# Kernel optimization log

Hardware: AMD Instinct MI355X
Metric: run time of the kernel (lower is better)

## Reference

```python
import jax, jax.numpy as jnp
import numpy as np

SLOPE = 25.0  # snntorch surrogate.fast_sigmoid default slope
THR = 1.0
BETA = 0.5
NUM_HEADS = 8

@jax.custom_vjp
def spike(u):
    # forward: heaviside; backward: fast-sigmoid surrogate
    return (u > 0).astype(u.dtype)

def _spike_fwd(u):
    return (u > 0).astype(u.dtype), u

def _spike_bwd(u, g):
    return (g / (SLOPE * jnp.abs(u) + 1.0) ** 2,)

spike.defvjp(_spike_fwd, _spike_bwd)

def lif(inp, mem):
    # snntorch Leaky, reset_mechanism='subtract': reset from previous mem (detached)
    reset = jax.lax.stop_gradient((mem > THR).astype(mem.dtype))
    mem_new = BETA * mem + inp - reset * THR
    spk = spike(mem_new - THR)
    return spk, mem_new

def conv1x1(x, W):
    # nn.Conv2d(C,C,1,bias=False): pure channel matmul
    return jnp.einsum('bihw,oi->bohw', x, W)

def setup_inputs():
    key = jax.random.key(0)
    ks = jax.random.split(key, 5)
    B, C, H, W = 8, 256, 64, 64
    x = jax.random.normal(ks[0], (B, C, H, W), jnp.float32)
    z = jnp.zeros((B, C, H, W), jnp.float32)
    s = 1.0 / np.sqrt(C)
    Wq = jax.random.normal(ks[1], (C, C), jnp.float32) * s
    Wk = jax.random.normal(ks[2], (C, C), jnp.float32) * s
    Wv = jax.random.normal(ks[3], (C, C), jnp.float32) * s
    Wo = jax.random.normal(ks[4], (C, C), jnp.float32) * s
    gamma = jnp.ones((C,), jnp.float32)
    beta_bn = jnp.zeros((C,), jnp.float32)
    return {'x': x, 'q_mem': z, 'k_mem': z, 'v_mem': z,
            'Wq': Wq, 'Wk': Wk, 'Wv': Wv, 'Wo': Wo,
            'gamma': gamma, 'beta_bn': beta_bn}

def reference(x, q_mem, k_mem, v_mem, Wq, Wk, Wv, Wo, gamma, beta_bn):
    B, C, H, W = x.shape
    N = H * W
    hd = C // NUM_HEADS
    scale = hd ** -0.5

    q_spk, q_mem_n = lif(conv1x1(x, Wq), q_mem)
    k_spk, k_mem_n = lif(conv1x1(x, Wk), k_mem)
    v_spk, v_mem_n = lif(conv1x1(x, Wv), v_mem)

    # bipolar spikes in {-1,+1}, reshape to (B, h, N, d)
    def to_heads(s):
        t = (2.0 * s - 1.0).reshape(B, NUM_HEADS, hd, N)
        return jnp.transpose(t, (0, 1, 3, 2))

    q = jax.nn.elu(to_heads(q_spk)) + 1.0
    k = jax.nn.elu(to_heads(k_spk)) + 1.0
    v = to_heads(v_spk)

    kv = jnp.einsum('bhnd,bhne->bhde', k, v)            # (B,h,d,d)
    out = jnp.einsum('bhnd,bhde->bhne', q, kv) * scale  # (B,h,N,d)
    k_sum = jnp.sum(k, axis=2)                          # (B,h,d)
    denom = jnp.einsum('bhnd,bhd->bhn', q, k_sum) + 1e-6
    out = out / denom[..., None]

    out = jnp.transpose(out, (0, 1, 3, 2)).reshape(B, C, H, W)
    out = conv1x1(out, Wo)

    # BatchNorm2d, training mode (biased batch stats), eps=1e-5
    mean = jnp.mean(out, axis=(0, 2, 3), keepdims=True)
    var = jnp.var(out, axis=(0, 2, 3), keepdims=True)
    out = (out - mean) / jnp.sqrt(var + 1e-5)
    out = out * gamma[None, :, None, None] + beta_bn[None, :, None, None]

    return (out, q_mem_n, k_mem_n, v_mem_n)
```

## Files before the change

kernel.cpp:

```cpp
#include <hip/hip_runtime.h>

#define B_ 8
#define C_ 256
#define N_ 4096
#define HD_ 32

#define ALPHA_ 0.36787944117144233f
#define BETAS_ (2.0f - ALPHA_)
#define SCALE_ 0.17677669529663687f

typedef _Float16 f16;
typedef _Float16 f16x8 __attribute__((ext_vector_type(8)));
typedef float f32x4 __attribute__((ext_vector_type(4)));
typedef unsigned long long u64;
typedef __attribute__((address_space(3))) f16 lds_f16;

#define MFMA(a,b,c) __builtin_amdgcn_mfma_f32_16x16x32_f16((a),(b),(c),0,0,0)

#define GLDS(g, l) __builtin_amdgcn_global_load_lds( \
    (const __attribute__((address_space(1))) void*)(g), \
    (__attribute__((address_space(3))) void*)(l), 16, 0, 0)

#define DSR(dst, off) asm volatile("ds_read_b128 %0, %1" : "=v"(dst) : "v"(off))

#define GLA(dst, ptr, ofs) asm volatile( \
    "global_load_dwordx4 %0, %1, off offset:%c2" \
    : "=v"(dst) : "v"(ptr), "i"(ofs))

template<int N> __device__ __forceinline__ void wait_vmcnt() {
    if constexpr (N == 0)       asm volatile("s_waitcnt vmcnt(0)" ::: "memory");
    else if constexpr (N == 2)  asm volatile("s_waitcnt vmcnt(2)" ::: "memory");
    else if constexpr (N == 4)  asm volatile("s_waitcnt vmcnt(4)" ::: "memory");
    else if constexpr (N == 6)  asm volatile("s_waitcnt vmcnt(6)" ::: "memory");
    else if constexpr (N == 8)  asm volatile("s_waitcnt vmcnt(8)" ::: "memory");
    else if constexpr (N == 12) asm volatile("s_waitcnt vmcnt(12)" ::: "memory");
    else if constexpr (N == 16) asm volatile("s_waitcnt vmcnt(16)" ::: "memory");
}

__global__ __launch_bounds__(256) void transpose_split(
    const float* __restrict__ x, f16* __restrict__ XTh, f16* __restrict__ XTl)
{
    __shared__ float tile[32][257];
    int t = threadIdx.x;
    int b = blockIdx.z, i0 = blockIdx.y * 32, n0 = blockIdx.x * 256;
    const float* src = x + ((size_t)b * C_ + i0) * N_ + n0;
    int r = t >> 3, c0 = (t & 7) * 32;
    #pragma unroll
    for (int q = 0; q < 8; ++q) {
        float4 v = *reinterpret_cast<const float4*>(src + (size_t)r * N_ + c0 + q * 4);
        tile[r][c0 + q*4 + 0] = v.x; tile[r][c0 + q*4 + 1] = v.y;
        tile[r][c0 + q*4 + 2] = v.z; tile[r][c0 + q*4 + 3] = v.w;
    }
    __syncthreads();
    size_t ob = ((size_t)b * N_ + n0 + t) * C_ + i0;
    #pragma unroll
    for (int q = 0; q < 4; ++q) {
        f16x8 hv, lv;
        #pragma unroll
        for (int j = 0; j < 8; ++j) {
            float v = tile[q*8 + j][t];
            f16 h = (f16)v;
            hv[j] = h;
            lv[j] = (f16)(v - (float)h);
        }
        *reinterpret_cast<f16x8*>(XTh + ob + q*8) = hv;
        *reinterpret_cast<f16x8*>(XTl + ob + q*8) = lv;
    }
}

__global__ __launch_bounds__(256) void weight_split(
    const float* __restrict__ Wq, const float* __restrict__ Wk,
    const float* __restrict__ Wv, const float* __restrict__ Wo,
    f16* __restrict__ Wch, f16* __restrict__ Wcl)
{
    int idx4 = (blockIdx.x * 256 + threadIdx.x) * 4;
    int o = idx4 >> 8, i = idx4 & 255;
    const float* src = (o < 256) ? (Wq + (size_t)o * 256)
                     : (o < 512) ? (Wk + (size_t)(o - 256) * 256)
                     : (o < 768) ? (Wv + (size_t)(o - 512) * 256)
                                 : (Wo + (size_t)(o - 768) * 256);
    float4 v = *reinterpret_cast<const float4*>(src + i);
    f16 h0 = (f16)v.x, h1 = (f16)v.y, h2 = (f16)v.z, h3 = (f16)v.w;
    f16 hh[4] = { h0, h1, h2, h3 };
    f16 ll[4] = { (f16)(v.x - (float)h0), (f16)(v.y - (float)h1),
                  (f16)(v.z - (float)h2), (f16)(v.w - (float)h3) };
    *reinterpret_cast<uint2*>(Wch + idx4) = *reinterpret_cast<uint2*>(hh);
    *reinterpret_cast<uint2*>(Wcl + idx4) = *reinterpret_cast<uint2*>(ll);
}

template<bool LIF, bool FULLP>
__global__ __launch_bounds__(256, 2) void mfma_gemm(
    const f16* __restrict__ Wch, const f16* __restrict__ Wcl,
    const f16* __restrict__ Bh,  const f16* __restrict__ Bl,
    const float* __restrict__ mq, const float* __restrict__ mk2,
    const float* __restrict__ mv,
    float* __restrict__ o0, float* __restrict__ o1, float* __restrict__ o2,
    u64* __restrict__ rowAll, float2* __restrict__ part)
{
    constexpr int SLOTS = FULLP ? 1024 : 512;
    constexpr int NGL   = FULLP ? 4 : 2;
    constexpr int NA    = FULLP ? 8 : 4;

    int gid = blockIdx.x;
    int b = gid & 7, slot = gid >> 3;
    int conv, oTi, nt;
    if (LIF) { conv = slot % 3; int rest = slot / 3; oTi = rest & 1; nt = rest >> 1; }
    else     { conv = 0;        oTi = slot & 1;      nt = slot >> 1; }
    int wRow0 = (LIF ? conv * 256 : 768) + oTi * 128;
    int chOut0 = oTi * 128;
    int nT = nt * 128;

    const float* memP = nullptr; float* outP; u64* rowP = nullptr;
    if (LIF) {
        memP = (conv == 0) ? mq : (conv == 1) ? mk2 : mv;
        outP = (conv == 0) ? o0 : (conv == 1) ? o1 : o2;
        rowP = rowAll + (size_t)conv * (8 * 256 * 64);
    } else outP = o0;

    __shared__ __align__(16) f16 smem[3][SLOTS * 8];

    int t = threadIdx.x;
    int wid = t >> 6, lane = t & 63;
    int wm = wid >> 1, wn = wid & 1;
    int lr = lane & 15, g = lane >> 4;

    const f16* gB[NGL];
    #pragma unroll
    for (int i = 0; i < NGL; ++i) {
        int s = i * 256 + t;
        int sp = s & 511;
        int r = sp >> 2, c = (sp & 3) ^ ((r >> 1) & 3);
        const f16* plane = (s < 512) ? Bh : Bl;
        gB[i] = plane + ((size_t)b * N_ + nT + r) * 256 + c * 8;
    }

    const f16* aPh[4]; const f16* aPl[4];
    #pragma unroll
    for (int m = 0; m < 4; ++m) {
        int off = (wRow0 + wm * 64 + m * 16 + lr) * 256 + g * 8;
        aPh[m] = Wch + off;
        aPl[m] = Wcl + off;
    }

    unsigned lbase = (unsigned)(size_t)(lds_f16*)&smem[0][0];
    unsigned offB[4];
    #pragma unroll
    for (int n = 0; n < 4; ++n) {
        int r = wn * 64 + n * 16 + lr;
        offB[n] = (unsigned)((r * 4 + (g ^ ((r >> 1) & 3))) * 16);
    }

    f32x4 acc[4][4];
    #pragma unroll
    for (int m = 0; m < 4; ++m)
        #pragma unroll
        for (int n = 0; n < 4; ++n) acc[m][n] = (f32x4){0.f, 0.f, 0.f, 0.f};

    f16x8 aH[2][4], aL[2][4];

    #pragma unroll
    for (int i = 0; i < NGL; ++i) GLDS(gB[i], &smem[0][(i * 256 + t) * 8]);
    #pragma unroll
    for (int m = 0; m < 4; ++m) {
        GLA(aH[0][m], aPh[m], 0);
        if (FULLP) GLA(aL[0][m], aPl[m], 0);
    }
    #pragma unroll
    for (int i = 0; i < NGL; ++i) GLDS(gB[i] + 32, &smem[1][(i * 256 + t) * 8]);
    wait_vmcnt<NGL>();
    __builtin_amdgcn_s_barrier();
    __builtin_amdgcn_sched_barrier(0);

#define GEMM_STEP(KS) do { \
    constexpr int ks = (KS); \
    constexpr int cur = ks & 1, nxt = (ks + 1) & 1; \
     \
    const unsigned base = lbase + (unsigned)((ks % 3) * (SLOTS * 16)); \
    f16x8 bhf[4], blf[4]; \
    _Pragma("unroll") \
    for (int n = 0; n < 4; ++n) { \
        DSR(bhf[n], base + offB[n]); \
        if (FULLP) DSR(blf[n], base + offB[n] + 8192); \
    } \
    __builtin_amdgcn_sched_barrier(0); \
     \
    if constexpr (ks < 7) { \
        _Pragma("unroll") \
        for (int m = 0; m < 4; ++m) { \
            GLA(aH[nxt][m], aPh[m], (ks + 1) * 64); \
            if (FULLP) GLA(aL[nxt][m], aPl[m], (ks + 1) * 64); \
        } \
    } \
    __builtin_amdgcn_sched_barrier(0); \
     \
    if constexpr (ks < 6) { \
        _Pragma("unroll") \
        for (int i = 0; i < NGL; ++i) \
            GLDS(gB[i] + (ks + 2) * 32, &smem[(ks + 2) % 3][(i * 256 + t) * 8]); \
    } \
    __builtin_amdgcn_sched_barrier(0); \
    asm volatile("s_waitcnt lgkmcnt(0)" ::: "memory"); \
    __builtin_amdgcn_sched_barrier(0); \
     \
    wait_vmcnt<(ks <= 5) ? (2 * NGL + NA) : (ks == 6 ? (NGL + NA) : 0)>(); \
    __builtin_amdgcn_sched_barrier(0); \
    _Pragma("unroll") \
    for (int n = 0; n < 4; ++n) \
        _Pragma("unroll") \
        for (int m = 0; m < 4; ++m) { \
            acc[m][n] = MFMA(aH[cur][m], bhf[n], acc[m][n]); \
            if (FULLP) { \
                acc[m][n] = MFMA(aH[cur][m], blf[n], acc[m][n]); \
                acc[m][n] = MFMA(aL[cur][m], bhf[n], acc[m][n]); \
            } \
        } \
    __builtin_amdgcn_sched_barrier(0); \
    if constexpr (ks < 7) { \
         \
        wait_vmcnt<(ks <= 5) ? (NA + NGL) : NA>(); \
        __builtin_amdgcn_s_barrier(); \
        __builtin_amdgcn_sched_barrier(0); \
    } \
} while (0)

    GEMM_STEP(0); GEMM_STEP(1); GEMM_STEP(2); GEMM_STEP(3);
    GEMM_STEP(4); GEMM_STEP(5); GEMM_STEP(6); GEMM_STEP(7);
#undef GEMM_STEP

    if (LIF) {
        #pragma unroll
        for (int m = 0; m < 4; ++m) {
            int oLoc = chOut0 + wm * 64 + m * 16 + g * 4;
            u64 rw0 = 0, rw1 = 0, rw2 = 0, rw3 = 0;
            #pragma unroll
            for (int n = 0; n < 4; ++n) {
                int nn = nT + wn * 64 + n * 16 + lr;
                #pragma unroll
                for (int r = 0; r < 4; ++r) {
                    size_t idx = ((size_t)b * C_ + oLoc + r) * N_ + nn;
                    float mm = memP[idx];
                    float v = 0.5f * mm + acc[m][n][r] - (mm > 1.0f ? 1.0f : 0.0f);
                    outP[idx] = v;
                    u64 bl = __ballot(v > 1.0f);
                    u64 fld = ((bl >> (g * 16)) & 0xFFFFull) << (n * 16);
                    if (r == 0) rw0 |= fld; else if (r == 1) rw1 |= fld;
                    else if (r == 2) rw2 |= fld; else rw3 |= fld;
                }
            }
            if (lr == 0) {
                size_t rb = ((size_t)b * 256 + oLoc) * 64 + (nt * 2 + wn);
                rowP[rb]       = rw0;
                rowP[rb + 64]  = rw1;
                rowP[rb + 128] = rw2;
                rowP[rb + 192] = rw3;
            }
        }
    } else {
        #pragma unroll
        for (int m = 0; m < 4; ++m) {
            #pragma unroll
            for (int r = 0; r < 4; ++r) {
                int ch = chOut0 + wm * 64 + m * 16 + g * 4 + r;
                float s1 = 0.f, s2 = 0.f;
                #pragma unroll
                for (int n = 0; n < 4; ++n) {
                    int nn = nT + wn * 64 + n * 16 + lr;
                    size_t idx = ((size_t)b * C_ + ch) * N_ + nn;
                    float v = acc[m][n][r];
                    outP[idx] = v;
                    s1 += v; s2 += v * v;
                }
                #pragma unroll
                for (int w = 1; w < 16; w <<= 1) {
                    s1 += __shfl_xor(s1, w);
                    s2 += __shfl_xor(s2, w);
                }
                if (lr == 0)
                    part[((size_t)ch * 8 + b) * 64 + nt * 2 + wn] = make_float2(s1, s2);
            }
        }
    }
}

__global__ __launch_bounds__(256) void kv_kernel(
    const u64* __restrict__ krow, const u64* __restrict__ vrow,
    float* __restrict__ kvp, float* __restrict__ ksump)
{
    int bh = blockIdx.x;
    int b = bh >> 3, h = bh & 7;
    __shared__ u64 kr[32][65], vr[32][65];
    __shared__ float ck[32], cv[32];
    int t = threadIdx.x;
    {
        size_t base = ((size_t)b * 256 + h * HD_) * 64;
        #pragma unroll
        for (int j = 0; j < 8; ++j) {
            int idx = t * 8 + j;
            int d = idx >> 6, w = idx & 63;
            kr[d][w] = krow[base + idx];
            vr[d][w] = vrow[base + idx];
        }
    }
    __syncthreads();

    if (t < 32) {
        int c = 0;
        for (int w = 0; w < 64; ++w) c += __popcll(kr[t][w]);
        ck[t] = (float)c;
    } else if (t < 64) {
        int dd = t - 32, c = 0;
        for (int w = 0; w < 64; ++w) c += __popcll(vr[dd][w]);
        cv[dd] = (float)c;
    }
    __syncthreads();

    int d = t >> 3, e0 = (t & 7) * 4;
    #pragma unroll
    for (int j = 0; j < 4; ++j) {
        int e = e0 + j, P = 0;
        for (int w = 0; w < 64; ++w) P += __popcll(kr[d][w] & vr[e][w]);
        float skv = 2.0f * (float)P - ck[d];
        float sv  = 2.0f * cv[e] - 4096.0f;
        kvp[(size_t)bh * 1024 + d * 32 + e] = ALPHA_ * sv + BETAS_ * skv;
    }
    if ((t & 7) == 0)
        ksump[bh * 32 + d] = ALPHA_ * 4096.0f + BETAS_ * ck[d];
}

__global__ __launch_bounds__(256) void att_kernel(
    const u64* __restrict__ qrow, const float* __restrict__ kvp,
    const float* __restrict__ ksump, f16* __restrict__ ATh)
{
    int bh = blockIdx.y; int b = bh >> 3, h = bh & 7;
    int n0 = blockIdx.x * 256;

    __shared__ u64 qw[32][5];
    int t = threadIdx.x;
    if (t < 128) {
        int d2 = t >> 2, w4 = t & 3;
        qw[d2][w4] = qrow[((size_t)b * 256 + h * HD_ + d2) * 64 + (n0 >> 6) + w4];
    }
    __syncthreads();

    float q[32];
    #pragma unroll
    for (int d2 = 0; d2 < 32; ++d2)
        q[d2] = ((qw[d2][t >> 6] >> (t & 63)) & 1) ? 2.0f : ALPHA_;

    const float* ksb = ksump + bh * 32;
    float den = 1e-6f;
    #pragma unroll
    for (int d2 = 0; d2 < 32; ++d2) den += q[d2] * ksb[d2];
    float rden = SCALE_ / den;

    const float* kvb = kvp + (size_t)bh * 1024;
    size_t ob = ((size_t)b * N_ + n0 + t) * C_ + h * HD_;
    #pragma unroll
    for (int qq = 0; qq < 4; ++qq) {
        f16x8 hv;
        #pragma unroll
        for (int j = 0; j < 8; ++j) {
            int e = qq * 8 + j;
            float num = 0.0f;
            #pragma unroll
            for (int d2 = 0; d2 < 32; ++d2) num += q[d2] * kvb[d2 * 32 + e];
            hv[j] = (f16)(num * rden);
        }
        *reinterpret_cast<f16x8*>(ATh + ob + qq * 8) = hv;
    }
}

__global__ __launch_bounds__(256) void bn_stats(
    const float2* __restrict__ part, float* __restrict__ stats)
{
    int o = blockIdx.x, t = threadIdx.x;
    float2 a = part[(size_t)o * 512 + t];
    float2 c = part[(size_t)o * 512 + 256 + t];
    double s = (double)a.x + (double)c.x;
    double ss = (double)a.y + (double)c.y;
    __shared__ double rs[256], rss[256];
    rs[t] = s; rss[t] = ss;
    __syncthreads();
    for (int st = 128; st > 0; st >>= 1) {
        if (t < st) { rs[t] += rs[t + st]; rss[t] += rss[t + st]; }
        __syncthreads();
    }
    if (t == 0) {
        double mean = rs[0] / 32768.0;
        double var  = rss[0] / 32768.0 - mean * mean;
        stats[o * 2 + 0] = (float)mean;
        stats[o * 2 + 1] = (float)(1.0 / sqrt(var + 1e-5));
    }
}

__global__ __launch_bounds__(256) void bn_apply(
    float* __restrict__ out, const float* __restrict__ stats,
    const float* __restrict__ gamma, const float* __restrict__ beta)
{
    size_t i = ((size_t)blockIdx.x * 256 + threadIdx.x) * 4;
    int o = (int)((i >> 12) & 255);
    float m = stats[o * 2], r = stats[o * 2 + 1];
    float g = gamma[o] * r;
    float c = beta[o] - m * g;
    float4 v = *reinterpret_cast<float4*>(&out[i]);
    v.x = v.x * g + c; v.y = v.y * g + c;
    v.z = v.z * g + c; v.w = v.w * g + c;
    *reinterpret_cast<float4*>(&out[i]) = v;
}

extern "C" void kernel_launch(void* const* d_in, const int* in_sizes, int n_in,
                              void* d_out, int out_size, void* d_ws, size_t ws_size,
                              hipStream_t stream)
{
    (void)in_sizes; (void)n_in; (void)out_size; (void)ws_size;

    const float* x     = (const float*)d_in[0];
    const float* qmem  = (const float*)d_in[1];
    const float* kmem  = (const float*)d_in[2];
    const float* vmem  = (const float*)d_in[3];
    const float* Wq    = (const float*)d_in[4];
    const float* Wk    = (const float*)d_in[5];
    const float* Wv    = (const float*)d_in[6];
    const float* Wo    = (const float*)d_in[7];
    const float* gamma = (const float*)d_in[8];
    const float* beta  = (const float*)d_in[9];

    const size_t TSZ = (size_t)B_ * C_ * N_;
    float* out0 = (float*)d_out;
    float* outq = out0 + TSZ;
    float* outk = outq + TSZ;
    float* outv = outk + TSZ;

    const size_t RSZ = (size_t)8 * 256 * 64;
    char* w = (char*)d_ws;
    f16* XTh = (f16*)w;           w += TSZ * 2;
    f16* XTl = (f16*)w;           w += TSZ * 2;
    f16* ATh = (f16*)w;           w += TSZ * 2;
    f16* Wch = (f16*)w;           w += 1024 * 256 * 2;
    f16* Wcl = (f16*)w;           w += 1024 * 256 * 2;
    u64* rowm = (u64*)w;          w += 3 * RSZ * 8;
    float2* part = (float2*)w;    w += 256 * 8 * 64 * 8;
    float* kvp   = (float*)w;     w += 64 * 1024 * 4;
    float* ksump = (float*)w;     w += 64 * 32 * 4;
    float* stats = (float*)w;     w += 256 * 2 * 4;

    dim3 blk(256);

    transpose_split<<<dim3(16, 8, 8), blk, 0, stream>>>(x, XTh, XTl);
    weight_split<<<dim3(256), blk, 0, stream>>>(Wq, Wk, Wv, Wo, Wch, Wcl);

    mfma_gemm<true, true><<<dim3(1536), blk, 0, stream>>>(
        Wch, Wcl, XTh, XTl, qmem, kmem, vmem, outq, outk, outv, rowm, nullptr);

    kv_kernel<<<dim3(64), blk, 0, stream>>>(rowm + RSZ, rowm + 2 * RSZ, kvp, ksump);

    att_kernel<<<dim3(16, 64), blk, 0, stream>>>(rowm, kvp, ksump, ATh);

    mfma_gemm<false, false><<<dim3(512), blk, 0, stream>>>(
        Wch, Wcl, ATh, ATh, nullptr, nullptr, nullptr, out0, nullptr, nullptr,
        nullptr, part);

    bn_stats<<<dim3(256), blk, 0, stream>>>(part, stats);
    bn_apply<<<dim3(8192), blk, 0, stream>>>(out0, stats, gamma, beta);
}
```

Measured before the change: 177.7 us.

## Give each wave private LDS B tiles to remove block barriers in GEMM

The GEMM main loop now has each wave load its own 64-row slice of the B operand into a wave-private, double-buffered LDS region, using a new XOR swizzle that interleaves the hi and lo planes. Because no wave reads another wave's data, the per-step s_barrier is dropped and the only synchronization left is vmcnt waits. The A-fragment and B prefetch now issue after the MFMAs for the step, two steps ahead. The cost is that B rows are duplicated across the wm wave pairs, which doubles global-to-LDS traffic and changes LDS size and occupancy.

```diff
diff --git a/kernel.cpp b/kernel.cpp
--- a/kernel.cpp
+++ b/kernel.cpp
@@ -29,11 +29,7 @@
 
 template<int N> __device__ __forceinline__ void wait_vmcnt() {
     if constexpr (N == 0)       asm volatile("s_waitcnt vmcnt(0)" ::: "memory");
-    else if constexpr (N == 2)  asm volatile("s_waitcnt vmcnt(2)" ::: "memory");
-    else if constexpr (N == 4)  asm volatile("s_waitcnt vmcnt(4)" ::: "memory");
-    else if constexpr (N == 6)  asm volatile("s_waitcnt vmcnt(6)" ::: "memory");
     else if constexpr (N == 8)  asm volatile("s_waitcnt vmcnt(8)" ::: "memory");
-    else if constexpr (N == 12) asm volatile("s_waitcnt vmcnt(12)" ::: "memory");
     else if constexpr (N == 16) asm volatile("s_waitcnt vmcnt(16)" ::: "memory");
 }
 
@@ -97,8 +93,9 @@
     float* __restrict__ o0, float* __restrict__ o1, float* __restrict__ o2,
     u64* __restrict__ rowAll, float2* __restrict__ part)
 {
-    constexpr int SLOTS = FULLP ? 1024 : 512;
-    constexpr int NGL   = FULLP ? 4 : 2;
+    constexpr int CH    = FULLP ? 8 : 4;
+    constexpr int SLOTB = FULLP ? 8192 : 4096;
+    constexpr int NGL   = FULLP ? 8 : 4;
     constexpr int NA    = FULLP ? 8 : 4;
 
     int gid = blockIdx.x;
@@ -117,21 +114,27 @@
         rowP = rowAll + (size_t)conv * (8 * 256 * 64);
     } else outP = o0;
 
-    __shared__ __align__(16) f16 smem[3][SLOTS * 8];
+    __shared__ __align__(16) char smem[4 * 2 * SLOTB];
 
     int t = threadIdx.x;
     int wid = t >> 6, lane = t & 63;
     int wm = wid >> 1, wn = wid & 1;
     int lr = lane & 15, g = lane >> 4;
 
+    const unsigned wbase = (unsigned)(wid * 2 * SLOTB);
+
     const f16* gB[NGL];
     #pragma unroll
     for (int i = 0; i < NGL; ++i) {
-        int s = i * 256 + t;
-        int sp = s & 511;
-        int r = sp >> 2, c = (sp & 3) ^ ((r >> 1) & 3);
-        const f16* plane = (s < 512) ? Bh : Bl;
-        gB[i] = plane + ((size_t)b * N_ + nT + r) * 256 + c * 8;
+        int s = i * 64 + lane;
+        int r, dc;
+        if (FULLP) { r = s >> 3; dc = (s & 7) ^ (r & 7); }
+        else       { r = s >> 2; dc = (s & 3) ^ (r & 3); }
+        const f16* plane;
+        int kc;
+        if (FULLP) { plane = (dc & 1) ? Bl : Bh; kc = dc >> 1; }
+        else       { plane = Bh;                 kc = dc; }
+        gB[i] = plane + ((size_t)b * N_ + nT + wn * 64 + r) * 256 + kc * 8;
     }
 
     const f16* aPh[4]; const f16* aPl[4];
@@ -142,12 +145,17 @@
         aPl[m] = Wcl + off;
     }
 
-    unsigned lbase = (unsigned)(size_t)(lds_f16*)&smem[0][0];
-    unsigned offB[4];
+    unsigned lbase = (unsigned)(size_t)(lds_f16*)&smem[0];
+    unsigned offBh[4], offBl[4];
     #pragma unroll
     for (int n = 0; n < 4; ++n) {
-        int r = wn * 64 + n * 16 + lr;
-        offB[n] = (unsigned)((r * 4 + (g ^ ((r >> 1) & 3))) * 16);
+        int rB = n * 16 + lr;
+        if (FULLP) {
+            offBh[n] = (unsigned)(rB * 128 + (((2 * g)     ^ (rB & 7)) * 16));
+            offBl[n] = (unsigned)(rB * 128 + (((2 * g + 1) ^ (rB & 7)) * 16));
+        } else {
+            offBh[n] = (unsigned)(rB * 64 + ((g ^ (rB & 3)) * 16));
+        }
     }
 
     f32x4 acc[4][4];
@@ -159,50 +167,35 @@
     f16x8 aH[2][4], aL[2][4];
 
     #pragma unroll
-    for (int i = 0; i < NGL; ++i) GLDS(gB[i], &smem[0][(i * 256 + t) * 8]);
+    for (int i = 0; i < NGL; ++i)
+        GLDS(gB[i], &smem[wbase + i * 1024]);
     #pragma unroll
     for (int m = 0; m < 4; ++m) {
         GLA(aH[0][m], aPh[m], 0);
         if (FULLP) GLA(aL[0][m], aPl[m], 0);
     }
     #pragma unroll
-    for (int i = 0; i < NGL; ++i) GLDS(gB[i] + 32, &smem[1][(i * 256 + t) * 8]);
-    wait_vmcnt<NGL>();
-    __builtin_amdgcn_s_barrier();
+    for (int i = 0; i < NGL; ++i)
+        GLDS(gB[i] + 32, &smem[wbase + SLOTB + i * 1024]);
+    #pragma unroll
+    for (int m = 0; m < 4; ++m) {
+        GLA(aH[1][m], aPh[m], 64);
+        if (FULLP) GLA(aL[1][m], aPl[m], 64);
+    }
+    wait_vmcnt<NGL + NA>();
     __builtin_amdgcn_sched_barrier(0);
 
 #define GEMM_STEP(KS) do { \
     constexpr int ks = (KS); \
-    constexpr int cur = ks & 1, nxt = (ks + 1) & 1; \
-     \
-    const unsigned base = lbase + (unsigned)((ks % 3) * (SLOTS * 16)); \
+    constexpr int cur = ks & 1; \
+    const unsigned bb = lbase + wbase + (unsigned)(cur * SLOTB); \
     f16x8 bhf[4], blf[4]; \
     _Pragma("unroll") \
     for (int n = 0; n < 4; ++n) { \
-        DSR(bhf[n], base + offB[n]); \
-        if (FULLP) DSR(blf[n], base + offB[n] + 8192); \
+        DSR(bhf[n], bb + offBh[n]); \
+        if (FULLP) DSR(blf[n], bb + offBl[n]); \
     } \
-    __builtin_amdgcn_sched_barrier(0); \
-     \
-    if constexpr (ks < 7) { \
-        _Pragma("unroll") \
-        for (int m = 0; m < 4; ++m) { \
-            GLA(aH[nxt][m], aPh[m], (ks + 1) * 64); \
-            if (FULLP) GLA(aL[nxt][m], aPl[m], (ks + 1) * 64); \
-        } \
-    } \
-    __builtin_amdgcn_sched_barrier(0); \
-     \
-    if constexpr (ks < 6) { \
-        _Pragma("unroll") \
-        for (int i = 0; i < NGL; ++i) \
-            GLDS(gB[i] + (ks + 2) * 32, &smem[(ks + 2) % 3][(i * 256 + t) * 8]); \
-    } \
-    __builtin_amdgcn_sched_barrier(0); \
     asm volatile("s_waitcnt lgkmcnt(0)" ::: "memory"); \
-    __builtin_amdgcn_sched_barrier(0); \
-     \
-    wait_vmcnt<(ks <= 5) ? (2 * NGL + NA) : (ks == 6 ? (NGL + NA) : 0)>(); \
     __builtin_amdgcn_sched_barrier(0); \
     _Pragma("unroll") \
     for (int n = 0; n < 4; ++n) \
@@ -215,12 +208,20 @@
             } \
         } \
     __builtin_amdgcn_sched_barrier(0); \
-    if constexpr (ks < 7) { \
-         \
-        wait_vmcnt<(ks <= 5) ? (NA + NGL) : NA>(); \
-        __builtin_amdgcn_s_barrier(); \
-        __builtin_amdgcn_sched_barrier(0); \
+    if constexpr (ks < 6) { \
+        _Pragma("unroll") \
+        for (int i = 0; i < NGL; ++i) \
+            GLDS(gB[i] + (ks + 2) * 32, &smem[wbase + cur * SLOTB + i * 1024]); \
+        _Pragma("unroll") \
+        for (int m = 0; m < 4; ++m) { \
+            GLA(aH[cur][m], aPh[m], (ks + 2) * 64); \
+            if (FULLP) GLA(aL[cur][m], aPl[m], (ks + 2) * 64); \
+        } \
     } \
+    __builtin_amdgcn_sched_barrier(0); \
+    if constexpr (ks < 6)      wait_vmcnt<NGL + NA>();  \
+    else if constexpr (ks == 6) wait_vmcnt<0>();         \
+    __builtin_amdgcn_sched_barrier(0); \
 } while (0)
 
     GEMM_STEP(0); GEMM_STEP(1); GEMM_STEP(2); GEMM_STEP(3);
```

Result: slower. 194.6 us (+9.5%).

## Stage weight tiles through LDS with 64x128 tiles and double buffering

Applied to the files above, without the earlier changes.

The GEMM kernels now use 64x128 output tiles instead of 128x128, which doubles the grid and raises the launch bound to three blocks per CU. Weight (A) fragments are no longer loaded per wave from global memory into registers; they are copied into LDS with global_load_lds next to the B tile, using an XOR swizzle. The three-stage B ring becomes a two-stage double buffer with a full vmcnt(0) wait before each barrier. This should cut register pressure and redundant weight loads and allow more occupancy, but each B tile is now fetched twice as often and less load latency is overlapped with compute.

```diff
diff --git a/kernel.cpp b/kernel.cpp
--- a/kernel.cpp
+++ b/kernel.cpp
@@ -23,18 +23,10 @@
 
 #define DSR(dst, off) asm volatile("ds_read_b128 %0, %1" : "=v"(dst) : "v"(off))
 
-#define GLA(dst, ptr, ofs) asm volatile( \
-    "global_load_dwordx4 %0, %1, off offset:%c2" \
-    : "=v"(dst) : "v"(ptr), "i"(ofs))
-
 template<int N> __device__ __forceinline__ void wait_vmcnt() {
     if constexpr (N == 0)       asm volatile("s_waitcnt vmcnt(0)" ::: "memory");
-    else if constexpr (N == 2)  asm volatile("s_waitcnt vmcnt(2)" ::: "memory");
-    else if constexpr (N == 4)  asm volatile("s_waitcnt vmcnt(4)" ::: "memory");
+    else if constexpr (N == 3)  asm volatile("s_waitcnt vmcnt(3)" ::: "memory");
     else if constexpr (N == 6)  asm volatile("s_waitcnt vmcnt(6)" ::: "memory");
-    else if constexpr (N == 8)  asm volatile("s_waitcnt vmcnt(8)" ::: "memory");
-    else if constexpr (N == 12) asm volatile("s_waitcnt vmcnt(12)" ::: "memory");
-    else if constexpr (N == 16) asm volatile("s_waitcnt vmcnt(16)" ::: "memory");
 }
 
 __global__ __launch_bounds__(256) void transpose_split(
@@ -89,7 +81,7 @@
 }
 
 template<bool LIF, bool FULLP>
-__global__ __launch_bounds__(256, 2) void mfma_gemm(
+__global__ __launch_bounds__(256, 3) void mfma_gemm(
     const f16* __restrict__ Wch, const f16* __restrict__ Wcl,
     const f16* __restrict__ Bh,  const f16* __restrict__ Bl,
     const float* __restrict__ mq, const float* __restrict__ mk2,
@@ -97,17 +89,20 @@
     float* __restrict__ o0, float* __restrict__ o1, float* __restrict__ o2,
     u64* __restrict__ rowAll, float2* __restrict__ part)
 {
-    constexpr int SLOTS = FULLP ? 1024 : 512;
-    constexpr int NGL   = FULLP ? 4 : 2;
-    constexpr int NA    = FULLP ? 8 : 4;
+    constexpr int CHA   = FULLP ? 8 : 4;
+    constexpr int CHL   = FULLP ? 3 : 2;
+    constexpr int ABYTE = 64 * CHA * 16;
+    constexpr int SLOTS = 192 * CHA;
+    constexpr int SLOTB = SLOTS * 16;
+    constexpr int NGL   = SLOTS / 256;
 
     int gid = blockIdx.x;
     int b = gid & 7, slot = gid >> 3;
     int conv, oTi, nt;
-    if (LIF) { conv = slot % 3; int rest = slot / 3; oTi = rest & 1; nt = rest >> 1; }
-    else     { conv = 0;        oTi = slot & 1;      nt = slot >> 1; }
-    int wRow0 = (LIF ? conv * 256 : 768) + oTi * 128;
-    int chOut0 = oTi * 128;
+    if (LIF) { conv = slot % 3; int rest = slot / 3; oTi = rest & 3; nt = rest >> 2; }
+    else     { conv = 0;        oTi = slot & 3;      nt = slot >> 2; }
+    int wRow0 = (LIF ? conv * 256 : 768) + oTi * 64;
+    int chOut0 = oTi * 64;
     int nT = nt * 128;
 
     const float* memP = nullptr; float* outP; u64* rowP = nullptr;
@@ -117,107 +112,100 @@
         rowP = rowAll + (size_t)conv * (8 * 256 * 64);
     } else outP = o0;
 
-    __shared__ __align__(16) f16 smem[3][SLOTS * 8];
+    __shared__ __align__(16) char smem[2][SLOTB];
 
     int t = threadIdx.x;
     int wid = t >> 6, lane = t & 63;
     int wm = wid >> 1, wn = wid & 1;
     int lr = lane & 15, g = lane >> 4;
 
-    const f16* gB[NGL];
+    const f16* gS[NGL];
     #pragma unroll
     for (int i = 0; i < NGL; ++i) {
         int s = i * 256 + t;
-        int sp = s & 511;
-        int r = sp >> 2, c = (sp & 3) ^ ((r >> 1) & 3);
-        const f16* plane = (s < 512) ? Bh : Bl;
-        gB[i] = plane + ((size_t)b * N_ + nT + r) * 256 + c * 8;
-    }
-
-    const f16* aPh[4]; const f16* aPl[4];
-    #pragma unroll
-    for (int m = 0; m < 4; ++m) {
-        int off = (wRow0 + wm * 64 + m * 16 + lr) * 256 + g * 8;
-        aPh[m] = Wch + off;
-        aPl[m] = Wcl + off;
+        const f16* gp;
+        if (s < 64 * CHA) {
+            int r = s >> CHL, dcl = (s & (CHA - 1)) ^ (r & (CHA - 1));
+            int kc = FULLP ? (dcl & 3) : dcl;
+            const f16* pl = (FULLP && (dcl >> 2)) ? Wcl : Wch;
+            gp = pl + (size_t)(wRow0 + r) * 256 + kc * 8;
+        } else {
+            int s2 = s - 64 * CHA;
+            int r = s2 >> CHL, dcl = (s2 & (CHA - 1)) ^ (r & (CHA - 1));
+            int kc = FULLP ? (dcl & 3) : dcl;
+            const f16* pl = (FULLP && (dcl >> 2)) ? Bl : Bh;
+            gp = pl + ((size_t)b * N_ + nT + r) * 256 + kc * 8;
+        }
+        gS[i] = gp;
     }
 
     unsigned lbase = (unsigned)(size_t)(lds_f16*)&smem[0][0];
-    unsigned offB[4];
+    unsigned offAh[2], offAl[2], offBh[4], offBl[4];
+    #pragma unroll
+    for (int m = 0; m < 2; ++m) {
+        int rA = wm * 32 + m * 16 + lr;
+        offAh[m] = (unsigned)((rA * CHA + (g ^ (rA & (CHA - 1)))) * 16);
+        if (FULLP)
+            offAl[m] = (unsigned)((rA * CHA + ((g + 4) ^ (rA & (CHA - 1)))) * 16);
+    }
     #pragma unroll
     for (int n = 0; n < 4; ++n) {
-        int r = wn * 64 + n * 16 + lr;
-        offB[n] = (unsigned)((r * 4 + (g ^ ((r >> 1) & 3))) * 16);
-    }
-
-    f32x4 acc[4][4];
-    #pragma unroll
-    for (int m = 0; m < 4; ++m)
+        int rB = wn * 64 + n * 16 + lr;
+        offBh[n] = (unsigned)(ABYTE + (rB * CHA + (g ^ (rB & (CHA - 1)))) * 16);
+        if (FULLP)
+            offBl[n] = (unsigned)(ABYTE + (rB * CHA + ((g + 4) ^ (rB & (CHA - 1)))) * 16);
+    }
+
+    f32x4 acc[2][4];
+    #pragma unroll
+    for (int m = 0; m < 2; ++m)
         #pragma unroll
         for (int n = 0; n < 4; ++n) acc[m][n] = (f32x4){0.f, 0.f, 0.f, 0.f};
 
-    f16x8 aH[2][4], aL[2][4];
-
-    #pragma unroll
-    for (int i = 0; i < NGL; ++i) GLDS(gB[i], &smem[0][(i * 256 + t) * 8]);
-    #pragma unroll
-    for (int m = 0; m < 4; ++m) {
-        GLA(aH[0][m], aPh[m], 0);
-        if (FULLP) GLA(aL[0][m], aPl[m], 0);
-    }
-    #pragma unroll
-    for (int i = 0; i < NGL; ++i) GLDS(gB[i] + 32, &smem[1][(i * 256 + t) * 8]);
-    wait_vmcnt<NGL>();
+    #pragma unroll
+    for (int i = 0; i < NGL; ++i)
+        GLDS(gS[i], &smem[0][(i * 256 + t) * 16]);
+    wait_vmcnt<0>();
     __builtin_amdgcn_s_barrier();
     __builtin_amdgcn_sched_barrier(0);
 
 #define GEMM_STEP(KS) do { \
     constexpr int ks = (KS); \
-    constexpr int cur = ks & 1, nxt = (ks + 1) & 1; \
-     \
-    const unsigned base = lbase + (unsigned)((ks % 3) * (SLOTS * 16)); \
-    f16x8 bhf[4], blf[4]; \
-    _Pragma("unroll") \
-    for (int n = 0; n < 4; ++n) { \
-        DSR(bhf[n], base + offB[n]); \
-        if (FULLP) DSR(blf[n], base + offB[n] + 8192); \
-    } \
-    __builtin_amdgcn_sched_barrier(0); \
+    constexpr int cur = ks & 1; \
      \
     if constexpr (ks < 7) { \
         _Pragma("unroll") \
-        for (int m = 0; m < 4; ++m) { \
-            GLA(aH[nxt][m], aPh[m], (ks + 1) * 64); \
-            if (FULLP) GLA(aL[nxt][m], aPl[m], (ks + 1) * 64); \
-        } \
+        for (int i = 0; i < NGL; ++i) \
+            GLDS(gS[i] + (ks + 1) * 32, &smem[cur ^ 1][(i * 256 + t) * 16]); \
     } \
     __builtin_amdgcn_sched_barrier(0); \
-     \
-    if constexpr (ks < 6) { \
-        _Pragma("unroll") \
-        for (int i = 0; i < NGL; ++i) \
-            GLDS(gB[i] + (ks + 2) * 32, &smem[(ks + 2) % 3][(i * 256 + t) * 8]); \
+    const unsigned bb = lbase + (unsigned)(cur * SLOTB); \
+    f16x8 ah[2], al[2], bhf[4], blf[4]; \
+    _Pragma("unroll") \
+    for (int m = 0; m < 2; ++m) { \
+        DSR(ah[m], bb + offAh[m]); \
+        if (FULLP) DSR(al[m], bb + offAl[m]); \
     } \
-    __builtin_amdgcn_sched_barrier(0); \
+    _Pragma("unroll") \
+    for (int n = 0; n < 4; ++n) { \
+        DSR(bhf[n], bb + offBh[n]); \
+        if (FULLP) DSR(blf[n], bb + offBl[n]); \
+    } \
     asm volatile("s_waitcnt lgkmcnt(0)" ::: "memory"); \
-    __builtin_amdgcn_sched_barrier(0); \
-     \
-    wait_vmcnt<(ks <= 5) ? (2 * NGL + NA) : (ks == 6 ? (NGL + NA) : 0)>(); \
     __builtin_amdgcn_sched_barrier(0); \
     _Pragma("unroll") \
     for (int n = 0; n < 4; ++n) \
         _Pragma("unroll") \
-        for (int m = 0; m < 4; ++m) { \
-            acc[m][n] = MFMA(aH[cur][m], bhf[n], acc[m][n]); \
+        for (int m = 0; m < 2; ++m) { \
+            acc[m][n] = MFMA(ah[m], bhf[n], acc[m][n]); \
             if (FULLP) { \
-                acc[m][n] = MFMA(aH[cur][m], blf[n], acc[m][n]); \
-                acc[m][n] = MFMA(aL[cur][m], bhf[n], acc[m][n]); \
+                acc[m][n] = MFMA(ah[m], blf[n], acc[m][n]); \
+                acc[m][n] = MFMA(al[m], bhf[n], acc[m][n]); \
             } \
         } \
     __builtin_amdgcn_sched_barrier(0); \
     if constexpr (ks < 7) { \
-         \
-        wait_vmcnt<(ks <= 5) ? (NA + NGL) : NA>(); \
+        wait_vmcnt<0>();                  \
         __builtin_amdgcn_s_barrier(); \
         __builtin_amdgcn_sched_barrier(0); \
     } \
@@ -229,8 +217,8 @@
 
     if (LIF) {
         #pragma unroll
-        for (int m = 0; m < 4; ++m) {
-            int oLoc = chOut0 + wm * 64 + m * 16 + g * 4;
+        for (int m = 0; m < 2; ++m) {
+            int oLoc = chOut0 + wm * 32 + m * 16 + g * 4;
             u64 rw0 = 0, rw1 = 0, rw2 = 0, rw3 = 0;
             #pragma unroll
             for (int n = 0; n < 4; ++n) {
@@ -257,10 +245,10 @@
         }
     } else {
         #pragma unroll
-        for (int m = 0; m < 4; ++m) {
+        for (int m = 0; m < 2; ++m) {
             #pragma unroll
             for (int r = 0; r < 4; ++r) {
-                int ch = chOut0 + wm * 64 + m * 16 + g * 4 + r;
+                int ch = chOut0 + wm * 32 + m * 16 + g * 4 + r;
                 float s1 = 0.f, s2 = 0.f;
                 #pragma unroll
                 for (int n = 0; n < 4; ++n) {
@@ -449,14 +437,14 @@
     transpose_split<<<dim3(16, 8, 8), blk, 0, stream>>>(x, XTh, XTl);
     weight_split<<<dim3(256), blk, 0, stream>>>(Wq, Wk, Wv, Wo, Wch, Wcl);
 
-    mfma_gemm<true, true><<<dim3(1536), blk, 0, stream>>>(
+    mfma_gemm<true, true><<<dim3(3072), blk, 0, stream>>>(
         Wch, Wcl, XTh, XTl, qmem, kmem, vmem, outq, outk, outv, rowm, nullptr);
 
     kv_kernel<<<dim3(64), blk, 0, stream>>>(rowm + RSZ, rowm + 2 * RSZ, kvp, ksump);
 
     att_kernel<<<dim3(16, 64), blk, 0, stream>>>(rowm, kvp, ksump, ATh);
 
-    mfma_gemm<false, false><<<dim3(512), blk, 0, stream>>>(
+    mfma_gemm<false, false><<<dim3(1024), blk, 0, stream>>>(
         Wch, Wcl, ATh, ATh, nullptr, nullptr, nullptr, out0, nullptr, nullptr,
         nullptr, part);
 
```

Result: faster. 151.3 us (-14.8%).
